# Performance work log

Measured on AMD Instinct MI355X. Metric: run time of the kernel, lower is better.

The kernel has to match this reference:

```python
import jax, jax.numpy as jnp
import numpy as np

TEMP = 0.1
DX = 64  # feature dim of x; W1 rows [0:DX] multiply x, rows [DX:] multiply y


def setup_inputs() -> dict:
    key = jax.random.key(0)
    k1, k2, k3, k4 = jax.random.split(key, 4)
    n, d, hidden = 1024, 64, 256
    x = jax.random.normal(k1, (n, d), dtype=jnp.float32)
    y = jax.random.normal(k2, (n, d), dtype=jnp.float32)
    W1 = jax.random.normal(k3, (2 * d, hidden), dtype=jnp.float32) * (1.0 / np.sqrt(2 * d))
    b1 = jnp.zeros((hidden,), dtype=jnp.float32)
    w2 = jax.random.normal(k4, (hidden,), dtype=jnp.float32) * (1.0 / np.sqrt(hidden))
    b2 = jnp.zeros((), dtype=jnp.float32)
    return {"x": x, "y": y, "W1": W1, "b1": b1, "w2": w2, "b2": b2}


def reference(x, y, W1, b1, w2, b2):
    n = y.shape[0]
    W1x, W1y = W1[:DX], W1[DX:]
    xp = x @ W1x                      # [n, hidden], indexed by j (x_tile[i,j] = x[j])
    yp = y @ W1y                      # [n, hidden], indexed by i (y_tile[i,j] = y[i])
    # Positive pairs: scorer(cat(x_i, y_i))
    pos = (jax.nn.relu(xp + yp + b1) @ w2 + b2) / TEMP          # [n]
    h = jax.nn.relu(yp[:, None, :] + xp[None, :, :] + b1)        # [n, n, hidden]
    scores = (h @ w2 + b2) / TEMP                                 # [n, n]
    lse = jax.nn.logsumexp(scores, axis=1)                        # [n]
    lower_bound = pos.mean() - (lse.mean() - jnp.log(jnp.float32(n)))
    return -lower_bound
```

## Files before the change

### kernel.cpp

```cpp
#include <hip/hip_runtime.h>
#include <math.h>

#define NN 1024
#define DD 64
#define HH 256
#define TEMP_INV 10.0f
#define KCH 64
#define NCH 4
#define NBLK2 256u

typedef float v2f __attribute__((ext_vector_type(2)));


__global__ __launch_bounds__(256)
void k1_proj(const float* __restrict__ x, const float* __restrict__ y,
             const float* __restrict__ W1, const float* __restrict__ b1,
             float* __restrict__ x2T, float* __restrict__ y2,
             float* __restrict__ E, float* __restrict__ gacc,
             unsigned int* __restrict__ tick)
{
    const int tid = threadIdx.x;
    if (blockIdx.x == 0) {
        *(float4*)&E[tid * 4] = make_float4(0.f, 0.f, 0.f, 0.f);
        if (tid == 0) { gacc[0] = 0.f; gacc[1] = 0.f; tick[0] = 0u; }
    }
    const int i0 = blockIdx.x * 2;
    float ax0 = 0.f, ax1 = 0.f, ay0 = 0.f, ay1 = 0.f;
    #pragma unroll 8
    for (int kk = 0; kk < DD; ++kk) {
        const float wx = W1[kk * HH + tid];
        const float wy = W1[(DD + kk) * HH + tid];
        ax0 = fmaf(x[i0 * DD + kk],       wx, ax0);
        ax1 = fmaf(x[(i0 + 1) * DD + kk], wx, ax1);
        ay0 = fmaf(y[i0 * DD + kk],       wy, ay0);
        ay1 = fmaf(y[(i0 + 1) * DD + kk], wy, ay1);
    }
    const float b1t = b1[tid];
    *(float2*)&x2T[tid * NN + i0] = make_float2(ax0 + b1t, ax1 + b1t);
    y2[i0 * HH + tid]       = ay0;
    y2[(i0 + 1) * HH + tid] = ay1;
}

__global__ __launch_bounds__(512, 4)
void k2_scores(const float* __restrict__ x2T, const float* __restrict__ y2,
               const float* __restrict__ w2, const float* __restrict__ b2,
               float* __restrict__ E, float* __restrict__ gacc,
               unsigned int* __restrict__ tick, float* __restrict__ out)
{
    __shared__ float xs[2][KCH][64];
    __shared__ float redf[256];
    __shared__ unsigned int s_old;
    const int t  = threadIdx.x;
    const int bj = blockIdx.x;
    const int bi = blockIdx.y;
    const int j0 = bj * 64;
    const int rr = t >> 5;
    const int cc = t & 31;
    const int rbase = bi * 64 + rr * 4;
    const float* yb = y2 + rbase * HH;

    const int wv  = t >> 6;
    const int ln  = t & 63;
    const int sro = ln >> 4;
    const int sco = (ln & 15) * 4;

    v2f acc[4];
    #pragma unroll
    for (int p = 0; p < 4; ++p) acc[p] = (v2f){0.f, 0.f};
    const v2f zero = {0.f, 0.f};

    #define STAGE(c, b)                                                        \
    {                                                                          \
        _Pragma("unroll")                                                      \
        for (int h = 0; h < 2; ++h) {                                          \
            const int row = wv * 8 + h * 4;                                    \
            const float* gsrc =                                               \
                &x2T[((c) * KCH + row + sro) * NN + j0 + sco];                 \
            __builtin_amdgcn_global_load_lds(                                  \
                (const __attribute__((address_space(1))) unsigned int*)gsrc,   \
                (__attribute__((address_space(3))) unsigned int*)&xs[b][row][0],\
                16, 0, 0);                                                     \
        }                                                                      \
    }

    STAGE(0, 0);
    for (int c = 0; c < NCH; ++c) {
        __syncthreads();
        if (c + 1 < NCH) STAGE(c + 1, (c + 1) & 1);
        const int cur = c & 1;
        #pragma unroll
        for (int g = 0; g < 16; ++g) {
            const int gg = c * 16 + g;
            float4 yv4[4];
            #pragma unroll
            for (int p = 0; p < 4; ++p)
                yv4[p] = *(const float4*)&yb[p * HH + gg * 4];
            #pragma unroll
            for (int e = 0; e < 4; ++e) {
                const float wk = w2[gg * 4 + e];
                const v2f wv2 = {wk, wk};
                const v2f xv = *(const v2f*)&xs[cur][g * 4 + e][cc * 2];
                #pragma unroll
                for (int p = 0; p < 4; ++p) {
                    const float yv = (e == 0) ? yv4[p].x : (e == 1) ? yv4[p].y
                                   : (e == 2) ? yv4[p].z : yv4[p].w;
                    v2f z = xv + (v2f){yv, yv};
                    z = __builtin_elementwise_max(z, zero);
                    acc[p] = z * wv2 + acc[p];
                }
            }
        }
    }
    #undef STAGE

    const float bb = b2[0];
    const v2f bbv = {bb, bb};
    v2f sc[4];
    #pragma unroll
    for (int p = 0; p < 4; ++p) sc[p] = (acc[p] + bbv) * TEMP_INV;

    const int col0 = j0 + cc * 2;
    float dv = 0.f; bool isd = false;
    #pragma unroll
    for (int p = 0; p < 4; ++p) {
        const int row = rbase + p;
        if (row == col0)     { dv += sc[p].x; isd = true; }
        if (row == col0 + 1) { dv += sc[p].y; isd = true; }
    }
    if (isd) atomicAdd(&gacc[1], dv);

    float e_[4];
    #pragma unroll
    for (int p = 0; p < 4; ++p)
        e_[p] = __expf(sc[p].x) + __expf(sc[p].y);
    #pragma unroll
    for (int mk = 16; mk >= 1; mk >>= 1) {
        #pragma unroll
        for (int p = 0; p < 4; ++p)
            e_[p] += __shfl_xor(e_[p], mk);
    }
    if (cc == 0) {
        #pragma unroll
        for (int p = 0; p < 4; ++p)
            atomicAdd(&E[rbase + p], e_[p]);
    }

    asm volatile("s_waitcnt vmcnt(0)" ::: "memory");
    __syncthreads();
    if (t == 0) s_old = atomicAdd(tick, 1u);
    __syncthreads();
    if (s_old == NBLK2 - 1u) {
        if (t < 256) {
            float ls = 0.f;
            #pragma unroll
            for (int r = 0; r < 4; ++r) {
                const float ev = __hip_atomic_load(&E[t + r * 256],
                                                   __ATOMIC_RELAXED,
                                                   __HIP_MEMORY_SCOPE_AGENT);
                ls += logf(ev);
            }
            redf[t] = ls;
        }
        __syncthreads();
        for (int s2 = 128; s2 > 0; s2 >>= 1) {
            if (t < s2) redf[t] += redf[t + s2];
            __syncthreads();
        }
        if (t == 0) {
            const float pos_sum = __hip_atomic_load(&gacc[1], __ATOMIC_RELAXED,
                                                    __HIP_MEMORY_SCOPE_AGENT);
            out[0] = redf[0] / (float)NN - logf((float)NN)
                   - pos_sum / (float)NN;
        }
    }
}

extern "C" void kernel_launch(void* const* d_in, const int* in_sizes, int n_in,
                              void* d_out, int out_size, void* d_ws, size_t ws_size,
                              hipStream_t stream)
{
    const float* x  = (const float*)d_in[0];
    const float* y  = (const float*)d_in[1];
    const float* W1 = (const float*)d_in[2];
    const float* b1 = (const float*)d_in[3];
    const float* w2 = (const float*)d_in[4];
    const float* b2 = (const float*)d_in[5];
    float* out = (float*)d_out;

    float* ws   = (float*)d_ws;
    float* x2T  = ws;
    float* y2   = x2T + HH * NN;
    float* E    = y2 + NN * HH;
    float* gacc = E + NN;
    unsigned int* tick = (unsigned int*)(gacc + 2);

    hipLaunchKernelGGL(k1_proj, dim3(NN / 2), dim3(256), 0, stream,
                       x, y, W1, b1, x2T, y2, E, gacc, tick);
    hipLaunchKernelGGL(k2_scores, dim3(16, 16), dim3(512), 0, stream,
                       x2T, y2, w2, b2, E, gacc, tick, out);
}
```

Baseline: 39.93 us.

## Shrink score tiles to 32x32 with 256-thread blocks and 2x2 per-thread outputs

Reduces the k2 tile from 64x64 with 512 threads to 32x32 with 256 threads, launching a 32x32 grid (1024 blocks) so all CUs get more blocks. Each thread now computes a 2x2 score patch with scalar fmaf instead of a 4x2 patch with packed v2f math. This aims for better load balance across the GPU's compute units, but lowers per-thread register reuse, doubles redundant y2/x2T reloads, and raises atomic traffic on E and the ticket counter.

```diff
diff --git a/kernel.cpp b/kernel.cpp
--- a/kernel.cpp
+++ b/kernel.cpp
@@ -7,9 +7,7 @@
 #define TEMP_INV 10.0f
 #define KCH 64
 #define NCH 4
-#define NBLK2 256u
-
-typedef float v2f __attribute__((ext_vector_type(2)));
+#define NBLK2 1024u
 
 
 __global__ __launch_bounds__(256)
@@ -41,39 +39,36 @@
     y2[(i0 + 1) * HH + tid] = ay1;
 }
 
-__global__ __launch_bounds__(512, 4)
+__global__ __launch_bounds__(256, 4)
 void k2_scores(const float* __restrict__ x2T, const float* __restrict__ y2,
                const float* __restrict__ w2, const float* __restrict__ b2,
                float* __restrict__ E, float* __restrict__ gacc,
                unsigned int* __restrict__ tick, float* __restrict__ out)
 {
-    __shared__ float xs[2][KCH][64];
+    __shared__ float xs[2][KCH][32];
     __shared__ float redf[256];
     __shared__ unsigned int s_old;
     const int t  = threadIdx.x;
     const int bj = blockIdx.x;
     const int bi = blockIdx.y;
-    const int j0 = bj * 64;
-    const int rr = t >> 5;
-    const int cc = t & 31;
-    const int rbase = bi * 64 + rr * 4;
+    const int j0 = bj * 32;
+    const int rr = t >> 4;
+    const int cc = t & 15;
+    const int rbase = bi * 32 + rr * 2;
     const float* yb = y2 + rbase * HH;
 
     const int wv  = t >> 6;
     const int ln  = t & 63;
-    const int sro = ln >> 4;
-    const int sco = (ln & 15) * 4;
+    const int sro = ln >> 3;
+    const int sco = (ln & 7) * 4;
 
-    v2f acc[4];
-    #pragma unroll
-    for (int p = 0; p < 4; ++p) acc[p] = (v2f){0.f, 0.f};
-    const v2f zero = {0.f, 0.f};
+    float a00 = 0.f, a01 = 0.f, a10 = 0.f, a11 = 0.f;
 
     #define STAGE(c, b)                                                        \
     {                                                                          \
         _Pragma("unroll")                                                      \
         for (int h = 0; h < 2; ++h) {                                          \
-            const int row = wv * 8 + h * 4;                                    \
+            const int row = wv * 16 + h * 8;                                   \
             const float* gsrc =                                               \
                 &x2T[((c) * KCH + row + sro) * NN + j0 + sco];                 \
             __builtin_amdgcn_global_load_lds(                                  \
@@ -91,58 +86,49 @@
         #pragma unroll
         for (int g = 0; g < 16; ++g) {
             const int gg = c * 16 + g;
-            float4 yv4[4];
-            #pragma unroll
-            for (int p = 0; p < 4; ++p)
-                yv4[p] = *(const float4*)&yb[p * HH + gg * 4];
+            const float4 y0 = *(const float4*)&yb[gg * 4];
+            const float4 y1 = *(const float4*)&yb[HH + gg * 4];
             #pragma unroll
             for (int e = 0; e < 4; ++e) {
                 const float wk = w2[gg * 4 + e];
-                const v2f wv2 = {wk, wk};
-                const v2f xv = *(const v2f*)&xs[cur][g * 4 + e][cc * 2];
-                #pragma unroll
-                for (int p = 0; p < 4; ++p) {
-                    const float yv = (e == 0) ? yv4[p].x : (e == 1) ? yv4[p].y
-                                   : (e == 2) ? yv4[p].z : yv4[p].w;
-                    v2f z = xv + (v2f){yv, yv};
-                    z = __builtin_elementwise_max(z, zero);
-                    acc[p] = z * wv2 + acc[p];
-                }
+                const float2 xv = *(const float2*)&xs[cur][g * 4 + e][cc * 2];
+                const float yv0 = (e == 0) ? y0.x : (e == 1) ? y0.y
+                                : (e == 2) ? y0.z : y0.w;
+                const float yv1 = (e == 0) ? y1.x : (e == 1) ? y1.y
+                                : (e == 2) ? y1.z : y1.w;
+                a00 = fmaf(fmaxf(yv0 + xv.x, 0.f), wk, a00);
+                a01 = fmaf(fmaxf(yv0 + xv.y, 0.f), wk, a01);
+                a10 = fmaf(fmaxf(yv1 + xv.x, 0.f), wk, a10);
+                a11 = fmaf(fmaxf(yv1 + xv.y, 0.f), wk, a11);
             }
         }
     }
     #undef STAGE
 
     const float bb = b2[0];
-    const v2f bbv = {bb, bb};
-    v2f sc[4];
-    #pragma unroll
-    for (int p = 0; p < 4; ++p) sc[p] = (acc[p] + bbv) * TEMP_INV;
+    const float s00 = (a00 + bb) * TEMP_INV;
+    const float s01 = (a01 + bb) * TEMP_INV;
+    const float s10 = (a10 + bb) * TEMP_INV;
+    const float s11 = (a11 + bb) * TEMP_INV;
 
     const int col0 = j0 + cc * 2;
     float dv = 0.f; bool isd = false;
-    #pragma unroll
-    for (int p = 0; p < 4; ++p) {
-        const int row = rbase + p;
-        if (row == col0)     { dv += sc[p].x; isd = true; }
-        if (row == col0 + 1) { dv += sc[p].y; isd = true; }
-    }
+    if (rbase == col0)         { dv += s00; isd = true; }
+    if (rbase == col0 + 1)     { dv += s01; isd = true; }
+    if (rbase + 1 == col0)     { dv += s10; isd = true; }
+    if (rbase + 1 == col0 + 1) { dv += s11; isd = true; }
     if (isd) atomicAdd(&gacc[1], dv);
 
-    float e_[4];
+    float e0 = __expf(s00) + __expf(s01);
+    float e1 = __expf(s10) + __expf(s11);
     #pragma unroll
-    for (int p = 0; p < 4; ++p)
-        e_[p] = __expf(sc[p].x) + __expf(sc[p].y);
-    #pragma unroll
-    for (int mk = 16; mk >= 1; mk >>= 1) {
-        #pragma unroll
-        for (int p = 0; p < 4; ++p)
-            e_[p] += __shfl_xor(e_[p], mk);
+    for (int mk = 8; mk >= 1; mk >>= 1) {
+        e0 += __shfl_xor(e0, mk);
+        e1 += __shfl_xor(e1, mk);
     }
     if (cc == 0) {
-        #pragma unroll
-        for (int p = 0; p < 4; ++p)
-            atomicAdd(&E[rbase + p], e_[p]);
+        atomicAdd(&E[rbase],     e0);
+        atomicAdd(&E[rbase + 1], e1);
     }
 
     asm volatile("s_waitcnt vmcnt(0)" ::: "memory");
@@ -150,17 +136,15 @@
     if (t == 0) s_old = atomicAdd(tick, 1u);
     __syncthreads();
     if (s_old == NBLK2 - 1u) {
-        if (t < 256) {
-            float ls = 0.f;
-            #pragma unroll
-            for (int r = 0; r < 4; ++r) {
-                const float ev = __hip_atomic_load(&E[t + r * 256],
-                                                   __ATOMIC_RELAXED,
-                                                   __HIP_MEMORY_SCOPE_AGENT);
-                ls += logf(ev);
-            }
-            redf[t] = ls;
+        float ls = 0.f;
+        #pragma unroll
+        for (int r = 0; r < 4; ++r) {
+            const float ev = __hip_atomic_load(&E[t + r * 256],
+                                               __ATOMIC_RELAXED,
+                                               __HIP_MEMORY_SCOPE_AGENT);
+            ls += logf(ev);
         }
+        redf[t] = ls;
         __syncthreads();
         for (int s2 = 128; s2 > 0; s2 >>= 1) {
             if (t < s2) redf[t] += redf[t + s2];
@@ -196,6 +180,6 @@
 
     hipLaunchKernelGGL(k1_proj, dim3(NN / 2), dim3(256), 0, stream,
                        x, y, W1, b1, x2T, y2, E, gacc, tick);
-    hipLaunchKernelGGL(k2_scores, dim3(16, 16), dim3(512), 0, stream,
+    hipLaunchKernelGGL(k2_scores, dim3(32, 32), dim3(256), 0, stream,
                        x2T, y2, w2, b2, E, gacc, tick, out);
 }
```

After: 41.95 us. 5.0% more time.
